# Kernel tuning notes

Hardware: AMD Instinct MI355X
Metric: run time of the kernel (lower is better)

The kernel has to match this reference:

```python
import jax, jax.numpy as jnp
import numpy as np

# Static configuration (matches init_kwargs)
L = 3264          # seq_length
K = 12            # ktc=4 -> K=12
LOCC = 4          # ktc=4 -> Locc=4
S, B, A = 8, 64, 4  # streams (user/port pairs), batch, rx antennas
DELAY_MIN, DELAY_MAX = -10, 10


def _phasor(m):
    # m: integer shifts [S, B] -> exp(1j*2*pi*m*n/L) as [S, B, L]
    n = jnp.arange(L, dtype=jnp.int32)
    ang = (2.0 * np.pi / L) * ((m[..., None] * n) % L).astype(jnp.float32)
    return jax.lax.complex(jnp.cos(ang), jnp.sin(ang))


def _linear_interp(h_avg):
    # np.interp with uniform source grid orig[i] = (LOCC-1)/2 + i*LOCC, clamped at ends.
    # h_avg: [S, B, A, R] complex, R = L // LOCC -> [S, B, A, L]
    R = L // LOCC
    new = jnp.arange(L, dtype=jnp.float32)
    t = jnp.clip((new - (LOCC - 1) / 2.0) / LOCC, 0.0, float(R - 1))
    i0 = jnp.floor(t).astype(jnp.int32)
    i1 = jnp.minimum(i0 + 1, R - 1)
    frac = (t - i0).astype(jnp.float32)
    return h_avg[..., i0] * (1.0 - frac) + h_avg[..., i1] * frac


def reference(ls_real, ls_imag, cyclic_shifts, noise_powers):
    ls = jax.lax.complex(ls_real, ls_imag)                     # [S,B,A,L]
    ideal_peak = ((K - cyclic_shifts) % K) * (L // K)          # [S]

    # Stage 1: IFFT + timing-offset search (torch.no_grad in original)
    h_time = jnp.fft.ifft(ls, axis=-1)
    power = jax.lax.stop_gradient(jnp.sum(jnp.abs(h_time) ** 2, axis=2))  # [S,B,L]
    offs = jnp.arange(DELAY_MIN, DELAY_MAX + 1, dtype=jnp.int32)          # [21]
    cand_idx = (ideal_peak[:, None] + offs[None, :]) % L                   # [S,21]
    cand_idx = jnp.broadcast_to(cand_idx[:, None, :], (S, B, offs.shape[0]))
    cand_pow = jnp.take_along_axis(power, cand_idx, axis=-1)               # [S,B,21]
    t_off = offs[jnp.argmax(cand_pow, axis=-1)]                            # [S,B]
    m = t_off + ideal_peak[:, None]                                        # [S,B]
    ph_m = _phasor(m)        # [S,B,L]
    ph_T = _phasor(t_off)    # [S,B,L]

    # Stage 2: phasor shift, OCC demux, interpolation (inside no_grad in original)
    h_shift = ls * ph_m[:, :, None, :]
    h_avg = h_shift.reshape(S, B, A, L // LOCC, LOCC).mean(-1)             # [S,B,A,L/4]
    h_interp = jax.lax.stop_gradient(_linear_interp(h_avg))                # [S,B,A,L]

    # Stage 3: global residual against stream (0,0)'s LS estimate
    total_recon = jnp.sum(h_interp * jnp.conj(ph_m)[:, :, None, :], axis=0)  # [B,A,L]
    residual = ls[0] - total_recon                                           # [B,A,L]

    # Stage 4: apply residual, MMSE (identity: mmse_module=None), timing recovery
    h_wr = h_interp + residual[None, :, :, None, :].squeeze(3) if False else h_interp + residual[None] * ph_m[:, :, None, :]
    final = h_wr * jnp.conj(ph_T)[:, :, None, :]                             # [S,B,A,L]
    return jnp.stack([final.real, final.imag]).astype(jnp.float32)          # [2,S,B,A,L]


def setup_inputs() -> dict:
    key = jax.random.key(0)
    k1, k2, k3, k4 = jax.random.split(key, 4)
    return {
        "ls_real": jax.random.normal(k1, (S, B, A, L), dtype=jnp.float32),
        "ls_imag": jax.random.normal(k2, (S, B, A, L), dtype=jnp.float32),
        "cyclic_shifts": jax.random.randint(k3, (S,), 0, K, dtype=jnp.int32),
        "noise_powers": jax.random.uniform(k4, (B,), dtype=jnp.float32),
    }
```

## Files before the change

### kernel.cpp

```cpp
#include <hip/hip_runtime.h>

namespace {

constexpr int L = 3264;
constexpr int K = 12;
constexpr int S = 8;
constexpr int B = 64;
constexpr int A = 4;
constexpr int R = 816;
constexpr int NOFF = 21;
constexpr int PEAK_STEP = L / K;
constexpr float TWO_PI = 6.28318530717958647692f;
constexpr float CINV = TWO_PI / (float)L;
constexpr int NCHUNK = (L + 255) / 256;
constexpr int HS_MAX = 66;

__device__ __forceinline__ float rfl(float x) {
    return __uint_as_float(__builtin_amdgcn_readfirstlane(__float_as_uint(x)));
}

__global__ __launch_bounds__(256)
void k_table(float2* __restrict__ tw)
{
    const int j = blockIdx.x * 256 + threadIdx.x;
    if (j < L) {
        float sv, cv;
        __sincosf(CINV * (float)j, &sv, &cv);
        tw[j] = make_float2(cv, sv);
    }
}

template <int NB>
__device__ __forceinline__ void dft_bins(
    const float* __restrict__ pr, const float* __restrict__ pi_,
    int idx0d0, int tid, int lane, int w, float2 (*red)[11])
{
    const int jb = (tid * idx0d0) % L;
    float br, bi; __sincosf(CINV * (float)jb, &bi, &br);
    float lr, li; __sincosf(CINV * (float)tid, &li, &lr);
    float pwr[NB], pwi[NB], ar[NB], ai[NB];
    pwr[0] = br; pwi[0] = bi;
    #pragma unroll
    for (int d = 1; d < NB; ++d) {
        pwr[d] = pwr[d-1] * lr - pwi[d-1] * li;
        pwi[d] = pwr[d-1] * li + pwi[d-1] * lr;
    }
    #pragma unroll
    for (int d = 0; d < NB; ++d) { ar[d] = 0.f; ai[d] = 0.f; }

    const int js = (256 * idx0d0) % L;
    float s0r, s0i; __sincosf(CINV * (float)js, &s0i, &s0r);
    float c8r, c8i; __sincosf(CINV * 256.0f, &c8i, &c8r);
    float str_[NB], sti_[NB];
    {
        float cr = s0r, ci = s0i;
        #pragma unroll
        for (int d = 0; d < NB; ++d) {
            str_[d] = rfl(cr); sti_[d] = rfl(ci);
            const float nr2 = cr * c8r - ci * c8i;
            ci = cr * c8i + ci * c8r;
            cr = nr2;
        }
    }

    float xr = pr[tid], xi = pi_[tid];
    for (int it = 0; it < 12; ++it) {
        float nxr = 0.f, nxi = 0.f;
        if (it < 11) {
            nxr = pr[tid + ((it + 1) << 8)];
            nxi = pi_[tid + ((it + 1) << 8)];
        } else if (tid < 192) {
            nxr = pr[tid + 3072];
            nxi = pi_[tid + 3072];
        }
        #pragma unroll
        for (int d = 0; d < NB; ++d) {
            ar[d] += xr * pwr[d] - xi * pwi[d];
            ai[d] += xr * pwi[d] + xi * pwr[d];
            const float nr2 = pwr[d] * str_[d] - pwi[d] * sti_[d];
            pwi[d] = pwr[d] * sti_[d] + pwi[d] * str_[d];
            pwr[d] = nr2;
        }
        xr = nxr; xi = nxi;
    }
    if (tid < 192) {
        #pragma unroll
        for (int d = 0; d < NB; ++d) {
            ar[d] += xr * pwr[d] - xi * pwi[d];
            ai[d] += xr * pwi[d] + xi * pwr[d];
        }
    }

    #pragma unroll
    for (int d = 0; d < NB; ++d) {
        float r = ar[d], im = ai[d];
        #pragma unroll
        for (int o = 32; o > 0; o >>= 1) {
            r  += __shfl_xor(r, o);
            im += __shfl_xor(im, o);
        }
        if (lane == 0) red[w][d] = make_float2(r, im);
    }
}

__global__ __launch_bounds__(256)
void k_dft(const float* __restrict__ lsr, const float* __restrict__ lsi,
           const int* __restrict__ cs, float* __restrict__ pow_out)
{
    __shared__ float2 red[4][11];

    const int blk = blockIdx.x;
    const int row = blk >> 1;
    const int half = blk & 1;
    const int sb = row >> 2;
    const int a = row & 3;
    const int s = sb >> 6;
    const int tid = threadIdx.x;
    const int lane = tid & 63;
    const int w = tid >> 6;

    const int ideal = ((K - cs[s]) % K) * PEAK_STEP;
    int idx0 = (ideal - 10) % L; if (idx0 < 0) idx0 += L;
    const int d0 = half ? 10 : 0;
    const int idx0d0 = (idx0 + d0) % L;

    const float* __restrict__ pr  = lsr + (size_t)row * L;
    const float* __restrict__ pi_ = lsi + (size_t)row * L;

    if (half) dft_bins<11>(pr, pi_, idx0d0, tid, lane, w, red);
    else      dft_bins<10>(pr, pi_, idx0d0, tid, lane, w, red);
    __syncthreads();

    const int NB = half ? 11 : 10;
    if (w == 0 && lane < NB) {
        float rr = 0.f, ii = 0.f;
        #pragma unroll
        for (int q = 0; q < 4; ++q) { rr += red[q][lane].x; ii += red[q][lane].y; }
        pow_out[sb * (NOFF * A) + (d0 + lane) * A + a] = rr * rr + ii * ii;
    }
}

__global__ __launch_bounds__(64)
void k_argmax(const float* __restrict__ pow_in, const int* __restrict__ cs,
              int* __restrict__ toff_out, int* __restrict__ m_out)
{
    const int sb = blockIdx.x;
    const int lane = threadIdx.x;
    const int s = sb >> 6;
    const int ideal = ((K - cs[s]) % K) * PEAK_STEP;

    float pw = -1.f;
    if (lane < NOFF) {
        const float4 p4 = *(const float4*)(pow_in + sb * (NOFF * A) + lane * A);
        pw = p4.x + p4.y + p4.z + p4.w;
    }
    float mx = pw;
    #pragma unroll
    for (int o = 32; o > 0; o >>= 1) mx = fmaxf(mx, __shfl_xor(mx, o));
    const unsigned long long msk = __ballot(pw == mx);
    const int argd = __ffsll(msk) - 1;
    if (lane == 0) {
        const int toff = argd - 10;
        toff_out[sb] = toff;
        m_out[sb]    = toff + ideal;
    }
}

__global__ __launch_bounds__(256)
void k_final(const float* __restrict__ lsr, const float* __restrict__ lsi,
             const int* __restrict__ toff_arr, const int* __restrict__ m_arr,
             const float2* __restrict__ tw, float* __restrict__ out)
{
    __shared__ float2 twl[L];
    __shared__ float2 hs[S][HS_MAX];
    __shared__ int mps[S], tfs[S];

    const int bid = blockIdx.x;
    const int chunk = bid % NCHUNK;
    const int ba = bid / NCHUNK;
    const int b = ba >> 2;
    const int a = ba & 3;
    const int tid = threadIdx.x;

    for (int j = tid; j < L; j += 256) twl[j] = tw[j];
    if (tid < S) {
        int mp = m_arr[tid * B + b] % L; if (mp < 0) mp += L;
        mps[tid] = mp;
        int tp = toff_arr[tid * B + b] % L; if (tp < 0) tp += L;
        tfs[tid] = tp;
    }
    __syncthreads();

    const int imin = max(0, chunk * 64 - 1);
    const int imax = min(R - 1, chunk * 64 + 64);
    const int cnt = imax - imin + 1;

    for (int t = tid; t < S * HS_MAX; t += 256) {
        const int s = t / HS_MAX;
        const int ii = t % HS_MAX;
        if (ii < cnt) {
            const int i = imin + ii;
            const int sb = s * B + b;
            const int mp = mps[s];
            const float2 emp = twl[mp];
            const float2 w0 = twl[(mp * (4 * i)) % L];
            const float4 xr = *(const float4*)(lsr + ((size_t)sb * A + a) * L + 4 * i);
            const float4 xi = *(const float4*)(lsi + ((size_t)sb * A + a) * L + 4 * i);
            float wr = w0.x, wi = w0.y;
            float are, aim, nr;
            are  = xr.x * wr - xi.x * wi;  aim  = xr.x * wi + xi.x * wr;
            nr = wr * emp.x - wi * emp.y;  wi = wr * emp.y + wi * emp.x;  wr = nr;
            are += xr.y * wr - xi.y * wi;  aim += xr.y * wi + xi.y * wr;
            nr = wr * emp.x - wi * emp.y;  wi = wr * emp.y + wi * emp.x;  wr = nr;
            are += xr.z * wr - xi.z * wi;  aim += xr.z * wi + xi.z * wr;
            nr = wr * emp.x - wi * emp.y;  wi = wr * emp.y + wi * emp.x;  wr = nr;
            are += xr.w * wr - xi.w * wi;  aim += xr.w * wi + xi.w * wr;
            hs[s][ii] = make_float2(are * 0.25f, aim * 0.25f);
        }
    }
    __syncthreads();

    const int l = chunk * 256 + tid;
    if (l >= L) return;

    float t2 = ((float)l - 1.5f) * 0.25f;
    t2 = fminf(fmaxf(t2, 0.0f), (float)(R - 1));
    const int i0 = (int)t2;
    const int i1 = min(i0 + 1, R - 1);
    const float frac = t2 - (float)i0;

    float hire[S], hiim[S], pmre[S], pmim[S];
    float rre = 0.f, rim = 0.f;

    #pragma unroll
    for (int s = 0; s < S; ++s) {
        const float2 wm = twl[(mps[s] * l) % L];
        const float2 h0 = hs[s][i0 - imin];
        const float2 h1 = hs[s][i1 - imin];
        const float hr = h0.x * (1.f - frac) + h1.x * frac;
        const float hi = h0.y * (1.f - frac) + h1.y * frac;
        hire[s] = hr; hiim[s] = hi; pmre[s] = wm.x; pmim[s] = wm.y;
        rre += hr * wm.x + hi * wm.y;
        rim += hi * wm.x - hr * wm.y;
    }

    const size_t off0 = ((size_t)(b * A + a)) * L + l;
    const float resre = lsr[off0] - rre;
    const float resim = lsi[off0] - rim;

    #pragma unroll
    for (int s = 0; s < S; ++s) {
        const float wre = hire[s] + resre * pmre[s] - resim * pmim[s];
        const float wim = hiim[s] + resre * pmim[s] + resim * pmre[s];
        const float2 wt = twl[(tfs[s] * l) % L];
        const float fre = wre * wt.x + wim * wt.y;
        const float fim = wim * wt.x - wre * wt.y;
        const size_t o = (((size_t)(s * B + b)) * A + a) * L + l;
        __builtin_nontemporal_store(fre, &out[o]);
        __builtin_nontemporal_store(fim, &out[(size_t)S * B * A * L + o]);
    }
}

}

extern "C" void kernel_launch(void* const* d_in, const int* in_sizes, int n_in,
                              void* d_out, int out_size, void* d_ws, size_t ws_size,
                              hipStream_t stream) {
    (void)in_sizes; (void)n_in; (void)out_size; (void)ws_size;
    const float* lsr = (const float*)d_in[0];
    const float* lsi = (const float*)d_in[1];
    const int*   cs  = (const int*)d_in[2];

    int* toff = (int*)d_ws;
    int* marr = toff + 512;
    float2* tw   = (float2*)((char*)d_ws + 4096);
    float*  powb = (float*)((char*)d_ws + 30720);

    k_table <<<NCHUNK, 256, 0, stream>>>(tw);
    k_dft   <<<S * B * A * 2, 256, 0, stream>>>(lsr, lsi, cs, powb);
    k_argmax<<<S * B, 64, 0, stream>>>(powb, cs, toff, marr);
    k_final <<<B * A * NCHUNK, 256, 0, stream>>>(lsr, lsi, toff, marr, tw,
                                                 (float*)d_out);
}
```

Before: 178.6 us.

## Precompute per-offset phasor tables and share LDS-staged rows in DFT kernel

The DFT kernel now uses one 512-thread block per row. The row is staged into LDS once and both bin groups compute from it, so global reads are no longer duplicated across two blocks. The final kernel stops copying a full twiddle table into LDS per block. Instead it reads precomputed global tables of phasors per timing offset and per ideal peak, and combines them with a complex multiply. This removes the per-block table load and the modulo indexing, but adds scattered global table reads and a larger table-generation kernel.

```diff
diff --git a/kernel.cpp b/kernel.cpp
--- a/kernel.cpp
+++ b/kernel.cpp
@@ -19,25 +19,38 @@
     return __uint_as_float(__builtin_amdgcn_readfirstlane(__float_as_uint(x)));
 }
 
+__device__ __forceinline__ float2 cmul(float2 a, float2 b) {
+    return make_float2(a.x * b.x - a.y * b.y, a.x * b.y + a.y * b.x);
+}
+
 __global__ __launch_bounds__(256)
-void k_table(float2* __restrict__ tw)
-{
-    const int j = blockIdx.x * 256 + threadIdx.x;
-    if (j < L) {
-        float sv, cv;
-        __sincosf(CINV * (float)j, &sv, &cv);
-        tw[j] = make_float2(cv, sv);
+void k_tables(const int* __restrict__ cs,
+              float2* __restrict__ phT, float2* __restrict__ phI)
+{
+    const int g = blockIdx.x * 256 + threadIdx.x;
+    if (g < NOFF * L) {
+        const int t = g / L, l = g - t * L;
+        int j = ((t - 10) * l) % L; if (j < 0) j += L;
+        float sv, cv; __sincosf(CINV * (float)j, &sv, &cv);
+        phT[g] = make_float2(cv, sv);
+    } else if (g < (NOFF + S) * L) {
+        const int q = g - NOFF * L;
+        const int s = q / L, l = q - s * L;
+        const int ideal = ((K - cs[s]) % K) * PEAK_STEP;
+        const int j = (ideal * l) % L;
+        float sv, cv; __sincosf(CINV * (float)j, &sv, &cv);
+        phI[q] = make_float2(cv, sv);
     }
 }
 
 template <int NB>
 __device__ __forceinline__ void dft_bins(
-    const float* __restrict__ pr, const float* __restrict__ pi_,
-    int idx0d0, int tid, int lane, int w, float2 (*red)[11])
-{
-    const int jb = (tid * idx0d0) % L;
+    const float* __restrict__ lscr, const float* __restrict__ lsci,
+    int idx0d0, int grouplane, int lane, int w, float2 (*red)[11])
+{
+    const int jb = (grouplane * idx0d0) % L;
     float br, bi; __sincosf(CINV * (float)jb, &bi, &br);
-    float lr, li; __sincosf(CINV * (float)tid, &li, &lr);
+    float lr, li; __sincosf(CINV * (float)grouplane, &li, &lr);
     float pwr[NB], pwi[NB], ar[NB], ai[NB];
     pwr[0] = br; pwi[0] = bi;
     #pragma unroll
@@ -63,16 +76,10 @@
         }
     }
 
-    float xr = pr[tid], xi = pi_[tid];
     for (int it = 0; it < 12; ++it) {
-        float nxr = 0.f, nxi = 0.f;
-        if (it < 11) {
-            nxr = pr[tid + ((it + 1) << 8)];
-            nxi = pi_[tid + ((it + 1) << 8)];
-        } else if (tid < 192) {
-            nxr = pr[tid + 3072];
-            nxi = pi_[tid + 3072];
-        }
+        const int k = grouplane + (it << 8);
+        const float xr = lscr[k];
+        const float xi = lsci[k];
         #pragma unroll
         for (int d = 0; d < NB; ++d) {
             ar[d] += xr * pwr[d] - xi * pwi[d];
@@ -81,9 +88,10 @@
             pwi[d] = pwr[d] * sti_[d] + pwi[d] * str_[d];
             pwr[d] = nr2;
         }
-        xr = nxr; xi = nxi;
-    }
-    if (tid < 192) {
+    }
+    if (grouplane < 192) {
+        const float xr = lscr[grouplane + 3072];
+        const float xi = lsci[grouplane + 3072];
         #pragma unroll
         for (int d = 0; d < NB; ++d) {
             ar[d] += xr * pwr[d] - xi * pwi[d];
@@ -103,51 +111,65 @@
     }
 }
 
-__global__ __launch_bounds__(256)
+__global__ __launch_bounds__(512)
 void k_dft(const float* __restrict__ lsr, const float* __restrict__ lsi,
            const int* __restrict__ cs, float* __restrict__ pow_out)
 {
-    __shared__ float2 red[4][11];
-
-    const int blk = blockIdx.x;
-    const int row = blk >> 1;
-    const int half = blk & 1;
+    __shared__ float lscr[L];
+    __shared__ float lsci[L];
+    __shared__ float2 red[8][11];
+
+    const int row = blockIdx.x;
     const int sb = row >> 2;
     const int a = row & 3;
     const int s = sb >> 6;
     const int tid = threadIdx.x;
     const int lane = tid & 63;
     const int w = tid >> 6;
+    const int grouplane = tid & 255;
+    const int grp = tid >> 8;
+
+    {
+        const float4* __restrict__ pr4 = (const float4*)(lsr + (size_t)row * L);
+        const float4* __restrict__ pi4 = (const float4*)(lsi + (size_t)row * L);
+        for (int idx = tid; idx < L / 4; idx += 512) {
+            const float4 r4 = pr4[idx];
+            const float4 i4 = pi4[idx];
+            ((float4*)lscr)[idx] = r4;
+            ((float4*)lsci)[idx] = i4;
+        }
+    }
+    __syncthreads();
 
     const int ideal = ((K - cs[s]) % K) * PEAK_STEP;
     int idx0 = (ideal - 10) % L; if (idx0 < 0) idx0 += L;
-    const int d0 = half ? 10 : 0;
+    const int d0 = grp ? 10 : 0;
     const int idx0d0 = (idx0 + d0) % L;
 
-    const float* __restrict__ pr  = lsr + (size_t)row * L;
-    const float* __restrict__ pi_ = lsi + (size_t)row * L;
-
-    if (half) dft_bins<11>(pr, pi_, idx0d0, tid, lane, w, red);
-    else      dft_bins<10>(pr, pi_, idx0d0, tid, lane, w, red);
+    if (grp) dft_bins<11>(lscr, lsci, idx0d0, grouplane, lane, w, red);
+    else     dft_bins<10>(lscr, lsci, idx0d0, grouplane, lane, w, red);
     __syncthreads();
 
-    const int NB = half ? 11 : 10;
-    if (w == 0 && lane < NB) {
+    if (tid < NOFF) {
+        const int d = tid;
+        const int g = (d < 10) ? 0 : 1;
+        const int dl = d - g * 10;
         float rr = 0.f, ii = 0.f;
         #pragma unroll
-        for (int q = 0; q < 4; ++q) { rr += red[q][lane].x; ii += red[q][lane].y; }
-        pow_out[sb * (NOFF * A) + (d0 + lane) * A + a] = rr * rr + ii * ii;
+        for (int q = 0; q < 4; ++q) {
+            rr += red[4 * g + q][dl].x;
+            ii += red[4 * g + q][dl].y;
+        }
+        pow_out[sb * (NOFF * A) + d * A + a] = rr * rr + ii * ii;
     }
 }
 
 __global__ __launch_bounds__(64)
 void k_argmax(const float* __restrict__ pow_in, const int* __restrict__ cs,
-              int* __restrict__ toff_out, int* __restrict__ m_out)
+              int* __restrict__ toff_out)
 {
     const int sb = blockIdx.x;
     const int lane = threadIdx.x;
-    const int s = sb >> 6;
-    const int ideal = ((K - cs[s]) % K) * PEAK_STEP;
 
     float pw = -1.f;
     if (lane < NOFF) {
@@ -159,21 +181,18 @@
     for (int o = 32; o > 0; o >>= 1) mx = fmaxf(mx, __shfl_xor(mx, o));
     const unsigned long long msk = __ballot(pw == mx);
     const int argd = __ffsll(msk) - 1;
-    if (lane == 0) {
-        const int toff = argd - 10;
-        toff_out[sb] = toff;
-        m_out[sb]    = toff + ideal;
-    }
+    if (lane == 0) toff_out[sb] = argd - 10;
 }
 
 __global__ __launch_bounds__(256)
 void k_final(const float* __restrict__ lsr, const float* __restrict__ lsi,
-             const int* __restrict__ toff_arr, const int* __restrict__ m_arr,
-             const float2* __restrict__ tw, float* __restrict__ out)
-{
-    __shared__ float2 twl[L];
+             const int* __restrict__ toff_arr,
+             const float2* __restrict__ phT, const float2* __restrict__ phI,
+             float* __restrict__ out)
+{
     __shared__ float2 hs[S][HS_MAX];
-    __shared__ int mps[S], tfs[S];
+    __shared__ float2 emp_s[S];
+    __shared__ int tfs[S];
 
     const int bid = blockIdx.x;
     const int chunk = bid % NCHUNK;
@@ -182,12 +201,10 @@
     const int a = ba & 3;
     const int tid = threadIdx.x;
 
-    for (int j = tid; j < L; j += 256) twl[j] = tw[j];
     if (tid < S) {
-        int mp = m_arr[tid * B + b] % L; if (mp < 0) mp += L;
-        mps[tid] = mp;
-        int tp = toff_arr[tid * B + b] % L; if (tp < 0) tp += L;
-        tfs[tid] = tp;
+        const int tf = toff_arr[tid * B + b] + 10;
+        tfs[tid] = tf;
+        emp_s[tid] = cmul(phI[tid * L + 1], phT[tf * L + 1]);
     }
     __syncthreads();
 
@@ -197,16 +214,15 @@
 
     for (int t = tid; t < S * HS_MAX; t += 256) {
         const int s = t / HS_MAX;
-        const int ii = t % HS_MAX;
+        const int ii = t - s * HS_MAX;
         if (ii < cnt) {
             const int i = imin + ii;
             const int sb = s * B + b;
-            const int mp = mps[s];
-            const float2 emp = twl[mp];
-            const float2 w0 = twl[(mp * (4 * i)) % L];
+            const float2 emp = emp_s[s];
+            float2 w2 = cmul(phI[s * L + 4 * i], phT[tfs[s] * L + 4 * i]);
             const float4 xr = *(const float4*)(lsr + ((size_t)sb * A + a) * L + 4 * i);
             const float4 xi = *(const float4*)(lsi + ((size_t)sb * A + a) * L + 4 * i);
-            float wr = w0.x, wi = w0.y;
+            float wr = w2.x, wi = w2.y;
             float are, aim, nr;
             are  = xr.x * wr - xi.x * wi;  aim  = xr.x * wi + xi.x * wr;
             nr = wr * emp.x - wi * emp.y;  wi = wr * emp.y + wi * emp.x;  wr = nr;
@@ -229,17 +245,20 @@
     const int i1 = min(i0 + 1, R - 1);
     const float frac = t2 - (float)i0;
 
-    float hire[S], hiim[S], pmre[S], pmim[S];
+    float hire[S], hiim[S], pmre[S], pmim[S], ptre[S], ptim[S];
     float rre = 0.f, rim = 0.f;
 
     #pragma unroll
     for (int s = 0; s < S; ++s) {
-        const float2 wm = twl[(mps[s] * l) % L];
+        const float2 pt = phT[tfs[s] * L + l];
+        const float2 wm = cmul(phI[s * L + l], pt);
         const float2 h0 = hs[s][i0 - imin];
         const float2 h1 = hs[s][i1 - imin];
         const float hr = h0.x * (1.f - frac) + h1.x * frac;
         const float hi = h0.y * (1.f - frac) + h1.y * frac;
-        hire[s] = hr; hiim[s] = hi; pmre[s] = wm.x; pmim[s] = wm.y;
+        hire[s] = hr; hiim[s] = hi;
+        pmre[s] = wm.x; pmim[s] = wm.y;
+        ptre[s] = pt.x; ptim[s] = pt.y;
         rre += hr * wm.x + hi * wm.y;
         rim += hi * wm.x - hr * wm.y;
     }
@@ -252,9 +271,8 @@
     for (int s = 0; s < S; ++s) {
         const float wre = hire[s] + resre * pmre[s] - resim * pmim[s];
         const float wim = hiim[s] + resre * pmim[s] + resim * pmre[s];
-        const float2 wt = twl[(tfs[s] * l) % L];
-        const float fre = wre * wt.x + wim * wt.y;
-        const float fim = wim * wt.x - wre * wt.y;
+        const float fre = wre * ptre[s] + wim * ptim[s];
+        const float fim = wim * ptre[s] - wre * ptim[s];
         const size_t o = (((size_t)(s * B + b)) * A + a) * L + l;
         __builtin_nontemporal_store(fre, &out[o]);
         __builtin_nontemporal_store(fim, &out[(size_t)S * B * A * L + o]);
@@ -272,13 +290,14 @@
     const int*   cs  = (const int*)d_in[2];
 
     int* toff = (int*)d_ws;
-    int* marr = toff + 512;
-    float2* tw   = (float2*)((char*)d_ws + 4096);
-    float*  powb = (float*)((char*)d_ws + 30720);
-
-    k_table <<<NCHUNK, 256, 0, stream>>>(tw);
-    k_dft   <<<S * B * A * 2, 256, 0, stream>>>(lsr, lsi, cs, powb);
-    k_argmax<<<S * B, 64, 0, stream>>>(powb, cs, toff, marr);
-    k_final <<<B * A * NCHUNK, 256, 0, stream>>>(lsr, lsi, toff, marr, tw,
+    float2* phT  = (float2*)((char*)d_ws + 4096);
+    float2* phI  = (float2*)((char*)d_ws + 4096 + 548352);
+    float*  powb = (float*)((char*)d_ws + 786432);
+
+    const int ntab = ((NOFF + S) * L + 255) / 256;
+    k_tables<<<ntab, 256, 0, stream>>>(cs, phT, phI);
+    k_dft   <<<S * B * A, 512, 0, stream>>>(lsr, lsi, cs, powb);
+    k_argmax<<<S * B, 64, 0, stream>>>(powb, cs, toff);
+    k_final <<<B * A * NCHUNK, 256, 0, stream>>>(lsr, lsi, toff, phT, phI,
                                                  (float*)d_out);
 }
```

Measured after the change: 186.0 us. 1.04x slower.
